# Optimization experiments

Measured on AMD Instinct MI355X. Metric: run time of the kernel, lower is better.

## Reference

```python
import jax, jax.numpy as jnp
import numpy as np

OUT_PLANES = 32
IN_PLANES = 16
PROD_DW = 256                      # prod_dw_in_planes
REP = PROD_DW // IN_PLANES         # 16
# group_list: deepcopy([4,4]); append(in_planes); reverse -> [16, 4, 4]
GROUP_LIST = [IN_PLANES, 4, 4]
B, H, W = 8, 32, 32


def setup_inputs() -> dict:
    key = jax.random.key(0)
    k1, k2, k3 = jax.random.split(key, 3)
    x = jax.random.normal(k1, (B, PROD_DW, H, W), dtype=jnp.float32)
    x2 = jax.random.normal(k2, (B, IN_PLANES, H, W), dtype=jnp.float32)
    # kaiming_normal_ on (512,1,1,1): fan_in = 1 -> std = sqrt(2)
    pw_weight = jax.random.normal(k3, (OUT_PLANES * IN_PLANES, 1, 1, 1), dtype=jnp.float32) * np.float32(np.sqrt(2.0))
    return {"x": x, "x2": x2, "pw_weight": pw_weight}


def reference(x, x2, pw_weight):
    b, c, h, w = x.shape
    w2 = pw_weight.reshape(OUT_PLANES, IN_PLANES)  # (o, i)
    # Grouped 1x1 conv with 1 channel per group == elementwise multiply.
    # Flattened channel order of out1 is (out, in, rep): weight index o*i repeated
    # REP times, input channel = (in*REP + r) = x channel g % PROD_DW.
    x4 = x.reshape(b, 1, IN_PLANES, REP, h, w)
    out1 = (x4 * w2[None, :, :, None, None, None]).reshape(b, OUT_PLANES * PROD_DW, h, w)
    # segment-sum over groups of IN_PLANES consecutive channels, then threshold gate
    summed_out1 = out1.reshape(b, -1, IN_PLANES, h, w).sum(axis=2)
    flag = (summed_out1 > 0).astype(out1.dtype)
    out1 = out1 * jnp.repeat(flag, IN_PLANES, axis=1)
    # hierarchical segment sums down to out_planes channels (check path in original)
    r = out1
    for g in GROUP_LIST:
        r = r.reshape(b, -1, g, h, w).sum(axis=2)
    relu_summed_out1 = r  # computed as in original (used only for the printed check)
    # dense 1x1 conv path
    out2 = jnp.einsum('bihw,oi->bohw', x2, w2)
    relu_out2 = jax.nn.relu(out2)
    return (out1, relu_out2)
```

## Files before the change

kernel.cpp:

```cpp
#include <hip/hip_runtime.h>

typedef float f4 __attribute__((ext_vector_type(4)));

constexpr int OUTP = 32;
constexpr int INP  = 16;
constexpr int REPS = 16;
constexpr int BB   = 8;
constexpr int HW   = 32 * 32;
constexpr int P4   = HW / 4;
constexpr size_t OUT1_F4 = (size_t)BB * OUTP * INP * REPS * P4;

__global__ __launch_bounds__(64) void qconv_pw_fused(
    const f4* __restrict__ x,
    const f4* __restrict__ x2,
    const float* __restrict__ w,
    f4* __restrict__ out)
{
    const int blk = blockIdx.x;
    const int tid = threadIdx.x;

    if (blk < 512) {
        const int chunk = blk & 3;
        const int bi    = blk >> 2;
        const int b     = bi >> 4;
        const int i     = bi & 15;
        const int v     = chunk * 64 + tid;

        const f4* xbase = x + (size_t)(b * 256 + i * REPS) * P4 + v;
        f4 xv[REPS];
#pragma unroll
        for (int r = 0; r < REPS; ++r) {
            xv[r] = xbase[(size_t)r * P4];
        }

        f4 S = (f4)(0.f);
#pragma unroll
        for (int r = 0; r < REPS; ++r) {
            S += xv[r];
        }

        for (int o = 0; o < OUTP; ++o) {
            const float wo = w[o * INP + i];
            f4 gw;
            gw.x = (wo * S.x > 0.f) ? wo : 0.f;
            gw.y = (wo * S.y > 0.f) ? wo : 0.f;
            gw.z = (wo * S.z > 0.f) ? wo : 0.f;
            gw.w = (wo * S.w > 0.f) ? wo : 0.f;

            const size_t base = (size_t)((b * OUTP + o) * INP + i) * REPS * P4 + v;
#pragma unroll
            for (int r = 0; r < REPS; ++r) {
                f4 res = xv[r] * gw;
                __builtin_nontemporal_store(res, &out[base + (size_t)r * P4]);
            }
        }
    } else {
        const int t    = (blk - 512) * 64 + tid;
        const int v    = t & (P4 - 1);
        const int rest = t >> 8;
        const int o    = rest & (OUTP - 1);
        const int b    = rest >> 5;

        const f4* xb = x2 + (size_t)(b * INP) * P4 + v;
        f4 acc = (f4)(0.f);
#pragma unroll
        for (int i = 0; i < INP; ++i) {
            const float wo = w[o * INP + i];
            acc += xb[(size_t)i * P4] * wo;
        }
        acc.x = fmaxf(acc.x, 0.f);
        acc.y = fmaxf(acc.y, 0.f);
        acc.z = fmaxf(acc.z, 0.f);
        acc.w = fmaxf(acc.w, 0.f);

        const size_t oidx = OUT1_F4 + (size_t)(b * OUTP + o) * P4 + v;
        __builtin_nontemporal_store(acc, &out[oidx]);
    }
}

extern "C" void kernel_launch(void* const* d_in, const int* in_sizes, int n_in,
                              void* d_out, int out_size, void* d_ws, size_t ws_size,
                              hipStream_t stream) {
    const f4* x  = (const f4*)d_in[0];
    const f4* x2 = (const f4*)d_in[1];
    const float* w = (const float*)d_in[2];
    f4* out = (f4*)d_out;

    const int grid = 512 + 1024;
    qconv_pw_fused<<<grid, 64, 0, stream>>>(x, x2, w, out);
}
```

Measured before the change: 282.5 us.

## Spread each rep over its own wave with LDS tree-reduce, drop nontemporal stores

Blocks grow from 64 to 1024 threads so each of the 16 reps is handled by a separate wave. The rep sum is formed with a shared-memory tree reduction across waves instead of one thread holding all 16 vectors in registers. Stores become plain writes rather than nontemporal ones, and the dense-conv path is remapped to 64 large blocks. The aim is to cut register pressure and raise parallelism on the store-bound out1 write, at the cost of several __syncthreads barriers and a different cache policy for a very large output.

```diff
diff --git a/kernel.cpp b/kernel.cpp
--- a/kernel.cpp
+++ b/kernel.cpp
@@ -10,12 +10,14 @@
 constexpr int P4   = HW / 4;
 constexpr size_t OUT1_F4 = (size_t)BB * OUTP * INP * REPS * P4;
 
-__global__ __launch_bounds__(64) void qconv_pw_fused(
+__global__ __launch_bounds__(1024) void qconv_pw_fused(
     const f4* __restrict__ x,
     const f4* __restrict__ x2,
     const float* __restrict__ w,
     f4* __restrict__ out)
 {
+    __shared__ f4 lds[REPS][64];
+
     const int blk = blockIdx.x;
     const int tid = threadIdx.x;
 
@@ -24,38 +26,35 @@
         const int bi    = blk >> 2;
         const int b     = bi >> 4;
         const int i     = bi & 15;
-        const int v     = chunk * 64 + tid;
+        const int r     = tid >> 6;
+        const int lane  = tid & 63;
+        const int v     = chunk * 64 + lane;
 
-        const f4* xbase = x + (size_t)(b * 256 + i * REPS) * P4 + v;
-        f4 xv[REPS];
+        const f4 xv = x[(size_t)(b * 256 + i * REPS + r) * P4 + v];
+
+        lds[r][lane] = xv;
+        __syncthreads();
+        f4 S = xv;
 #pragma unroll
-        for (int r = 0; r < REPS; ++r) {
-            xv[r] = xbase[(size_t)r * P4];
+        for (int k = 8; k >= 1; k >>= 1) {
+            if (r < k) { S += lds[r + k][lane]; lds[r][lane] = S; }
+            __syncthreads();
         }
+        S = lds[0][lane];
 
-        f4 S = (f4)(0.f);
+        const size_t base0 = (size_t)(((b * OUTP) * INP + i) * REPS + r) * P4 + v;
 #pragma unroll
-        for (int r = 0; r < REPS; ++r) {
-            S += xv[r];
-        }
-
         for (int o = 0; o < OUTP; ++o) {
             const float wo = w[o * INP + i];
-            f4 gw;
-            gw.x = (wo * S.x > 0.f) ? wo : 0.f;
-            gw.y = (wo * S.y > 0.f) ? wo : 0.f;
-            gw.z = (wo * S.z > 0.f) ? wo : 0.f;
-            gw.w = (wo * S.w > 0.f) ? wo : 0.f;
-
-            const size_t base = (size_t)((b * OUTP + o) * INP + i) * REPS * P4 + v;
-#pragma unroll
-            for (int r = 0; r < REPS; ++r) {
-                f4 res = xv[r] * gw;
-                __builtin_nontemporal_store(res, &out[base + (size_t)r * P4]);
-            }
+            f4 res;
+            res.x = (wo * S.x > 0.f) ? xv.x * wo : 0.f;
+            res.y = (wo * S.y > 0.f) ? xv.y * wo : 0.f;
+            res.z = (wo * S.z > 0.f) ? xv.z * wo : 0.f;
+            res.w = (wo * S.w > 0.f) ? xv.w * wo : 0.f;
+            out[base0 + (size_t)o * (INP * REPS * P4)] = res;
         }
     } else {
-        const int t    = (blk - 512) * 64 + tid;
+        const int t    = (blk - 512) * 1024 + tid;
         const int v    = t & (P4 - 1);
         const int rest = t >> 8;
         const int o    = rest & (OUTP - 1);
@@ -73,8 +72,7 @@
         acc.z = fmaxf(acc.z, 0.f);
         acc.w = fmaxf(acc.w, 0.f);
 
-        const size_t oidx = OUT1_F4 + (size_t)(b * OUTP + o) * P4 + v;
-        __builtin_nontemporal_store(acc, &out[oidx]);
+        out[OUT1_F4 + (size_t)(b * OUTP + o) * P4 + v] = acc;
     }
 }
 
@@ -86,6 +84,6 @@
     const float* w = (const float*)d_in[2];
     f4* out = (f4*)d_out;
 
-    const int grid = 512 + 1024;
-    qconv_pw_fused<<<grid, 64, 0, stream>>>(x, x2, w, out);
+    const int grid = 512 + 64;
+    qconv_pw_fused<<<grid, 1024, 0, stream>>>(x, x2, w, out);
 }
```

New measurement: 271.3 us. -4.0%, faster.

## Use 1024-thread blocks splitting reps across waves with LDS reduction

Applied to the files above, without the earlier changes.

Reworks the work split: each 1024-thread block handles one (batch, in-plane, quarter of outputs), with threads split over 4 rep groups and partial sums combined through shared memory. Grid shrinks from 1536 64-thread blocks to 576 1024-thread blocks, and register pressure per thread drops from 16 cached vectors to 4. Each block's stores now cover contiguous 16KB rows per output channel. The x slice is reloaded by 4 blocks per (b,i), and a barrier is added; the relu path stores become regular stores.

```diff
diff --git a/kernel.cpp b/kernel.cpp
--- a/kernel.cpp
+++ b/kernel.cpp
@@ -8,54 +8,60 @@
 constexpr int BB   = 8;
 constexpr int HW   = 32 * 32;
 constexpr int P4   = HW / 4;
-constexpr size_t OUT1_F4 = (size_t)BB * OUTP * INP * REPS * P4;
+constexpr int OSTRIDE_F4 = INP * REPS * P4;
+constexpr size_t OUT1_F4 = (size_t)BB * OUTP * OSTRIDE_F4;
 
-__global__ __launch_bounds__(64) void qconv_pw_fused(
+__global__ __launch_bounds__(1024, 8) void qconv_pw_fused(
     const f4* __restrict__ x,
     const f4* __restrict__ x2,
     const float* __restrict__ w,
     f4* __restrict__ out)
 {
+    __shared__ f4 lds[4][P4];
+
     const int blk = blockIdx.x;
     const int tid = threadIdx.x;
 
-    if (blk < 512) {
-        const int chunk = blk & 3;
-        const int bi    = blk >> 2;
-        const int b     = bi >> 4;
-        const int i     = bi & 15;
-        const int v     = chunk * 64 + tid;
+    if (blk >= 64) {
+        const int wu = blk - 64;
+        const int oq = wu & 3;
+        const int i  = (wu >> 2) & 15;
+        const int b  = wu >> 6;
+        const int r0 = tid >> 8;
+        const int v  = tid & 255;
 
         const f4* xbase = x + (size_t)(b * 256 + i * REPS) * P4 + v;
-        f4 xv[REPS];
+        f4 xv[4];
 #pragma unroll
-        for (int r = 0; r < REPS; ++r) {
-            xv[r] = xbase[(size_t)r * P4];
+        for (int k = 0; k < 4; ++k) {
+            xv[k] = xbase[(size_t)(r0 + 4 * k) * P4];
         }
 
-        f4 S = (f4)(0.f);
+        f4 part = xv[0] + xv[1] + xv[2] + xv[3];
+        lds[r0][v] = part;
+        __syncthreads();
+        f4 S = lds[0][v] + lds[1][v] + lds[2][v] + lds[3][v];
+
+        const size_t cbase = (size_t)(b * (OUTP * INP * REPS) + i * REPS) * P4;
+        const int j0 = r0 * P4 + v;
 #pragma unroll
-        for (int r = 0; r < REPS; ++r) {
-            S += xv[r];
-        }
-
-        for (int o = 0; o < OUTP; ++o) {
+        for (int oo = 0; oo < 8; ++oo) {
+            const int o = oq * 8 + oo;
             const float wo = w[o * INP + i];
             f4 gw;
             gw.x = (wo * S.x > 0.f) ? wo : 0.f;
             gw.y = (wo * S.y > 0.f) ? wo : 0.f;
             gw.z = (wo * S.z > 0.f) ? wo : 0.f;
             gw.w = (wo * S.w > 0.f) ? wo : 0.f;
-
-            const size_t base = (size_t)((b * OUTP + o) * INP + i) * REPS * P4 + v;
+            const size_t obase = cbase + (size_t)o * OSTRIDE_F4 + j0;
 #pragma unroll
-            for (int r = 0; r < REPS; ++r) {
-                f4 res = xv[r] * gw;
-                __builtin_nontemporal_store(res, &out[base + (size_t)r * P4]);
+            for (int k = 0; k < 4; ++k) {
+                f4 res = xv[k] * gw;
+                __builtin_nontemporal_store(res, &out[obase + (size_t)k * 1024]);
             }
         }
     } else {
-        const int t    = (blk - 512) * 64 + tid;
+        const int t    = blk * 1024 + tid;
         const int v    = t & (P4 - 1);
         const int rest = t >> 8;
         const int o    = rest & (OUTP - 1);
@@ -73,8 +79,7 @@
         acc.z = fmaxf(acc.z, 0.f);
         acc.w = fmaxf(acc.w, 0.f);
 
-        const size_t oidx = OUT1_F4 + (size_t)(b * OUTP + o) * P4 + v;
-        __builtin_nontemporal_store(acc, &out[oidx]);
+        out[OUT1_F4 + (size_t)(b * OUTP + o) * P4 + v] = acc;
     }
 }
 
@@ -86,6 +91,6 @@
     const float* w = (const float*)d_in[2];
     f4* out = (f4*)d_out;
 
-    const int grid = 512 + 1024;
-    qconv_pw_fused<<<grid, 64, 0, stream>>>(x, x2, w, out);
+    const int grid = 64 + 512;
+    qconv_pw_fused<<<grid, 1024, 0, stream>>>(x, x2, w, out);
 }
```

Measured after the change: 280.1 us. About the same (-0.8%).
